# Optimization experiments

Measured on AMD Instinct MI355X. Metric: run time of the kernel, lower is better.

## Reference

```python
import jax, jax.numpy as jnp
import numpy as np

BETA = 0.25
K = 4096
D = 256


def setup_inputs() -> dict:
    key = jax.random.key(0)
    k1, k2 = jax.random.split(key)
    z = jax.random.normal(k1, (4, D, 16, 32, 32), dtype=jnp.float32)
    # mimics nn.init.uniform_(embed.weight, -1/K, 1/K)
    embed = jax.random.uniform(k2, (K, D), minval=-1.0 / K, maxval=1.0 / K, dtype=jnp.float32)
    return {"z": z, "embed": embed}


def reference(z, embed):
    # z: [B, D, T, H, W] -> channel-last [B, T, H, W, D]
    z_perm = jnp.transpose(z, (0, 2, 3, 4, 1))
    flat = z_perm.reshape(-1, embed.shape[1])  # [N, D]
    # squared L2 distances via expansion: |z|^2 - 2 z.e + |e|^2  -> [N, K]
    dist = ((flat ** 2).sum(axis=1, keepdims=True)
            - 2.0 * flat @ embed.T
            + (embed ** 2).sum(axis=1)[None, :])
    idx = jnp.argmin(dist, axis=1)  # [N]
    z_q = embed[idx].reshape(z_perm.shape)  # [B, T, H, W, D]
    # straight-through estimator
    z_q_st = z_perm + jax.lax.stop_gradient(z_q - z_perm)
    z_q_st = jnp.transpose(z_q_st, (0, 4, 1, 2, 3))  # back to [B, D, T, H, W]
    e_q = jnp.transpose(z_q, (0, 4, 1, 2, 3))
    codebook_loss = jnp.mean((jax.lax.stop_gradient(e_q) - z) ** 2)
    commitment_loss = jnp.mean((e_q - jax.lax.stop_gradient(z)) ** 2)
    vq_loss = codebook_loss + BETA * commitment_loss
    indices = idx.reshape(z_perm.shape[:4])  # [B, T, H, W]
    return (z_q_st, vq_loss, indices)
```

## Files before the change

kernel.cpp:

```cpp
#include <hip/hip_runtime.h>
#include <float.h>

#define KC 4096
#define DIM 256
#define MB 16384
#define NTOT 65536
#define ZELEMS 16777216
#define LOSS_OFF 16777216
#define IDX_OFF  16777217
#define TAU 1.5e-4f

#define BT_OFF   524288
#define CNT_OFF  528400
#define CAND_OFF 532480
#define FULL_OFF 800000

typedef _Float16 h8 __attribute__((ext_vector_type(8)));
typedef float f4v __attribute__((ext_vector_type(4)));

__device__ __forceinline__ bool lexlt(float av, int ai, float bv, int bi) {
    return (av < bv) || (av == bv && ai < bi);
}

__global__ __launch_bounds__(256) void vq_prep(const float* __restrict__ e,
                                               float* __restrict__ out) {
    if (blockIdx.x < 512) {
        int t = blockIdx.x * 256 + threadIdx.x;
        int code = t >> 5, s8 = t & 31;
        const float4* src = reinterpret_cast<const float4*>(e + (size_t)code * DIM + s8 * 8);
        float4 v0 = src[0], v1 = src[1];
        float f[8] = {v0.x, v0.y, v0.z, v0.w, v1.x, v1.y, v1.z, v1.w};
        union { uint4 q; _Float16 h[8]; } P;
        #pragma unroll
        for (int p = 0; p < 8; ++p) P.h[p] = (_Float16)(f[p] * 4096.0f);
        int kc = s8 >> 2, khi = s8 & 3;
        int lane = khi * 16 + (code & 15);
        int slot = ((code >> 4) * 8 + kc) * 64 + lane;
        reinterpret_cast<uint4*>(out)[slot] = P.q;
    } else {
        int k = (blockIdx.x - 512) * 4 + (threadIdx.x >> 6);
        int lane = threadIdx.x & 63;
        float4 v = reinterpret_cast<const float4*>(e + (size_t)k * DIM)[lane];
        double s = (double)v.x * v.x + (double)v.y * v.y + (double)v.z * v.z + (double)v.w * v.w;
        #pragma unroll
        for (int off = 32; off > 0; off >>= 1) s += __shfl_down(s, off);
        if (lane == 0) out[BT_OFF + k] = (float)s;
    }
}

#define INS4(V0, V1, V2, V3, L0, L1, L2, L3, v, k)                              \
    if (v < V3) {                                                               \
        if (v < V2) {                                                           \
            V3 = V2; L3 = L2;                                                   \
            if (v < V1) {                                                       \
                V2 = V1; L2 = L1;                                               \
                if (v < V0) { V1 = V0; L1 = L0; V0 = v; L0 = k; }               \
                else        { V1 = v; L1 = k; }                                 \
            } else { V2 = v; L2 = k; }                                          \
        } else { V3 = v; L3 = k; }                                              \
    }

__global__ __launch_bounds__(256) void vq_fast(const float* __restrict__ z,
                                               float* __restrict__ out) {
    __shared__ uint4 etile[2][512];
    __shared__ unsigned long long lists[4][32][4];
    const int tid = threadIdx.x;
    const int wave = tid >> 6, lane = tid & 63;
    const int khi = lane >> 4, l16 = lane & 15;
    const int nbase = blockIdx.x * 128;
    const int b = nbase / MB;
    const int mbase = nbase % MB;
    const float* zb = z + (size_t)b * DIM * MB + mbase + wave * 32 + l16;

    h8 zf0[8], zf1[8];
    #pragma unroll
    for (int kc = 0; kc < 8; ++kc) {
        h8 va, vb;
        #pragma unroll
        for (int j = 0; j < 8; ++j) {
            size_t off = (size_t)(kc * 32 + khi * 8 + j) * MB;
            va[j] = (_Float16)zb[off];
            vb[j] = (_Float16)zb[off + 16];
        }
        zf0[kc] = va; zf1[kc] = vb;
    }

    const uint4* ET = reinterpret_cast<const uint4*>(out);
    const float* Btab = out + BT_OFF;

    float b10 = FLT_MAX, b11 = FLT_MAX;
    int bk0 = 0, bk1 = 0;
    float v00 = FLT_MAX, v01 = FLT_MAX, v02 = FLT_MAX, v03 = FLT_MAX;
    float v10 = FLT_MAX, v11 = FLT_MAX, v12 = FLT_MAX, v13 = FLT_MAX;
    int l00 = 0, l01 = 0, l02 = 0, l03 = 0;
    int l10 = 0, l11 = 0, l12 = 0, l13 = 0;

    uint4 r0 = ET[tid], r1 = ET[tid + 256];
    for (int tile = 0; tile < KC / 16; ++tile) {
        const int cur = tile & 1;
        etile[cur][tid] = r0; etile[cur][tid + 256] = r1;
        __syncthreads();
        if (tile < KC / 16 - 1) {
            r0 = ET[(size_t)(tile + 1) * 512 + tid];
            r1 = ET[(size_t)(tile + 1) * 512 + tid + 256];
        }

        f4v a0 = {0.f, 0.f, 0.f, 0.f}, a1 = a0;
        #pragma unroll
        for (int kc = 0; kc < 8; ++kc) {
            union { uint4 q; h8 v; } af;
            af.q = etile[cur][kc * 64 + lane];
            a0 = __builtin_amdgcn_mfma_f32_16x16x32_f16(af.v, zf0[kc], a0, 0, 0, 0);
            a1 = __builtin_amdgcn_mfma_f32_16x16x32_f16(af.v, zf1[kc], a1, 0, 0, 0);
        }

        const f4v Bv = *reinterpret_cast<const f4v*>(Btab + tile * 16 + khi * 4);
        const int kb = tile * 16 + khi * 4;
        float sc0[4], sc1[4];
        #pragma unroll
        for (int i = 0; i < 4; ++i) {
            sc0[i] = fmaf(-4.8828125e-4f, a0[i], Bv[i]);
            sc1[i] = fmaf(-4.8828125e-4f, a1[i], Bv[i]);
        }
        float m0 = fminf(fminf(sc0[0], sc0[1]), fminf(sc0[2], sc0[3]));
        if (m0 <= b10 + TAU) {
            #pragma unroll
            for (int i = 0; i < 4; ++i) {
                float s = sc0[i]; int k = kb + i;
                if (s < b10) {
                    if (b10 <= s + TAU) INS4(v00, v01, v02, v03, l00, l01, l02, l03, b10, bk0)
                    b10 = s; bk0 = k;
                } else if (s <= b10 + TAU) {
                    INS4(v00, v01, v02, v03, l00, l01, l02, l03, s, k)
                }
            }
        }
        float m1 = fminf(fminf(sc1[0], sc1[1]), fminf(sc1[2], sc1[3]));
        if (m1 <= b11 + TAU) {
            #pragma unroll
            for (int i = 0; i < 4; ++i) {
                float s = sc1[i]; int k = kb + i;
                if (s < b11) {
                    if (b11 <= s + TAU) INS4(v10, v11, v12, v13, l10, l11, l12, l13, b11, bk1)
                    b11 = s; bk1 = k;
                } else if (s <= b11 + TAU) {
                    INS4(v10, v11, v12, v13, l10, l11, l12, l13, s, k)
                }
            }
        }
    }

    float gb0 = b10, gb1 = b11;
    int gk0 = bk0, gk1 = bk1;
    #pragma unroll
    for (int off = 16; off < 64; off <<= 1) {
        float ov = __shfl_xor(gb0, off); int ok = __shfl_xor(gk0, off);
        if (lexlt(ov, ok, gb0, gk0)) { gb0 = ov; gk0 = ok; }
        ov = __shfl_xor(gb1, off); ok = __shfl_xor(gk1, off);
        if (lexlt(ov, ok, gb1, gk1)) { gb1 = ov; gk1 = ok; }
    }
    const float thr0 = gb0 + TAU, thr1 = gb1 + TAU;

    int n0 = 0, pa0 = 0, pb0 = 0, pc0 = 0, pd0 = 0;
    #define ADD0(kk) { if (n0 == 0) pa0 = kk; else if (n0 == 1) pb0 = kk; \
                       else if (n0 == 2) pc0 = kk; else if (n0 == 3) pd0 = kk; n0++; }
    if (b10 <= thr0) ADD0(bk0)
    if (v00 <= thr0) ADD0(l00)
    if (v01 <= thr0) ADD0(l01)
    if (v02 <= thr0) ADD0(l02)
    if (v03 <= thr0) ADD0(l03)
    int n1 = 0, pa1 = 0, pb1 = 0, pc1 = 0, pd1 = 0;
    #define ADD1(kk) { if (n1 == 0) pa1 = kk; else if (n1 == 1) pb1 = kk; \
                       else if (n1 == 2) pc1 = kk; else if (n1 == 3) pd1 = kk; n1++; }
    if (b11 <= thr1) ADD1(bk1)
    if (v10 <= thr1) ADD1(l10)
    if (v11 <= thr1) ADD1(l11)
    if (v12 <= thr1) ADD1(l12)
    if (v13 <= thr1) ADD1(l13)
    lists[wave][l16][khi] = ((unsigned long long)n0 << 48) |
        (unsigned long long)pa0 | ((unsigned long long)pb0 << 12) |
        ((unsigned long long)pc0 << 24) | ((unsigned long long)pd0 << 36);
    lists[wave][16 + l16][khi] = ((unsigned long long)n1 << 48) |
        (unsigned long long)pa1 | ((unsigned long long)pb1 << 12) |
        ((unsigned long long)pc1 << 24) | ((unsigned long long)pd1 << 36);
    __syncthreads();

    unsigned* cntg = (unsigned*)(out + CNT_OFF);
    #pragma unroll
    for (int set = 0; set < 2; ++set) {
        bool act = (lane < 16);
        int gidx = nbase + wave * 32 + set * 16 + l16;
        int I1 = set ? gk1 : gk0;
        int tot = 0, c[4];
        c[0] = c[1] = c[2] = c[3] = I1;
        if (act) {
            #pragma unroll
            for (int q = 0; q < 4; ++q) {
                unsigned long long pl = lists[wave][set * 16 + l16][q];
                int pc = (int)(pl >> 48);
                #pragma unroll
                for (int j = 0; j < 4; ++j) {
                    int kv = (int)((pl >> (12 * j)) & 4095ull);
                    if (j < pc && tot + j < 4) c[tot + j] = kv;
                }
                tot += pc;
            }
            out[IDX_OFF + gidx] = (float)I1;
        }
        bool cand = act && (tot >= 2) && (tot <= 4);
        bool full = act && (tot > 4);
        unsigned long long mc = __ballot(cand);
        if (mc) {
            int leader = __ffsll((long long)mc) - 1;
            unsigned base = 0;
            if (lane == leader) base = atomicAdd(cntg, (unsigned)__popcll(mc));
            base = __shfl(base, leader);
            if (cand) {
                unsigned pos = base + (unsigned)__popcll(mc & ((1ull << lane) - 1ull));
                reinterpret_cast<uint4*>(out + CAND_OFF)[pos] =
                    make_uint4((unsigned)gidx,
                               (unsigned)c[0] | ((unsigned)c[1] << 16),
                               (unsigned)c[2] | ((unsigned)c[3] << 16), 0u);
            }
        }
        unsigned long long mf = __ballot(full);
        if (mf) {
            int leader = __ffsll((long long)mf) - 1;
            unsigned base = 0;
            if (lane == leader) base = atomicAdd(cntg + 1, (unsigned)__popcll(mf));
            base = __shfl(base, leader);
            if (full) {
                unsigned pos = base + (unsigned)__popcll(mf & ((1ull << lane) - 1ull));
                reinterpret_cast<unsigned*>(out + FULL_OFF)[pos] = (unsigned)gidx;
            }
        }
    }
}

__global__ __launch_bounds__(256) void vq_resolve_cand(const float* __restrict__ z,
                                                       const float* __restrict__ e,
                                                       float* __restrict__ out) {
    const int wave = threadIdx.x >> 6, lane = threadIdx.x & 63;
    const unsigned n = *reinterpret_cast<const unsigned*>(out + CNT_OFF);
    const uint4* list = reinterpret_cast<const uint4*>(out + CAND_OFF);
    const float* Btab = out + BT_OFF;
    for (unsigned ei = blockIdx.x * 4 + wave; ei < n; ei += gridDim.x * 4) {
        uint4 ent = list[ei];
        const int gidx = (int)ent.x;
        const int c1 = (int)(ent.y & 0xFFFFu), c2 = (int)(ent.y >> 16);
        const int c3 = (int)(ent.z & 0xFFFFu), c4 = (int)(ent.z >> 16);
        const int b = gidx >> 14, m = gidx & (MB - 1);
        const float* zr = z + (size_t)b * DIM * MB + m;
        const float* e1 = e + (size_t)c1 * DIM;
        const float* e2 = e + (size_t)c2 * DIM;
        const float* e3 = e + (size_t)c3 * DIM;
        const float* e4 = e + (size_t)c4 * DIM;
        double A = 0.0;
        double d1 = 0.0, d2 = 0.0, d3 = 0.0, d4 = 0.0;
        #pragma unroll
        for (int jj = 0; jj < 4; ++jj) {
            int d = lane * 4 + jj;
            double zv = (double)zr[(size_t)d * MB];
            A = fma(zv, zv, A);
            d1 = fma(zv, (double)e1[d], d1);
            d2 = fma(zv, (double)e2[d], d2);
            d3 = fma(zv, (double)e3[d], d3);
            d4 = fma(zv, (double)e4[d], d4);
        }
        #pragma unroll
        for (int mm = 1; mm < 64; mm <<= 1) {
            A += __shfl_xor(A, mm);
            d1 += __shfl_xor(d1, mm); d2 += __shfl_xor(d2, mm);
            d3 += __shfl_xor(d3, mm); d4 += __shfl_xor(d4, mm);
        }
        if (lane == 0) {
            float Af = (float)A;
            float s1 = (Af - (float)(2.0 * d1)) + Btab[c1];
            float s2 = (Af - (float)(2.0 * d2)) + Btab[c2];
            float s3 = (Af - (float)(2.0 * d3)) + Btab[c3];
            float s4 = (Af - (float)(2.0 * d4)) + Btab[c4];
            float bv = s1; int bk = c1;
            if (lexlt(s2, c2, bv, bk)) { bv = s2; bk = c2; }
            if (lexlt(s3, c3, bv, bk)) { bv = s3; bk = c3; }
            if (lexlt(s4, c4, bv, bk)) { bv = s4; bk = c4; }
            out[IDX_OFF + gidx] = (float)bk;
        }
    }
}

__global__ __launch_bounds__(256) void vq_resolve_full(const float* __restrict__ z,
                                                       const float* __restrict__ e,
                                                       float* __restrict__ out) {
    __shared__ float zs[DIM];
    __shared__ float rv[4];
    __shared__ int ri[4];
    const int tid = threadIdx.x;
    const int wave = tid >> 6, lane = tid & 63;
    const unsigned n = reinterpret_cast<const unsigned*>(out + CNT_OFF)[1];
    const unsigned* list = reinterpret_cast<const unsigned*>(out + FULL_OFF);
    const float* Btab = out + BT_OFF;
    for (unsigned ei = blockIdx.x; ei < n; ei += gridDim.x) {
        const int gidx = (int)list[ei];
        const int b = gidx >> 14, m = gidx & (MB - 1);
        const float* zr = z + (size_t)b * DIM * MB + m;
        if (tid < DIM) zs[tid] = zr[(size_t)tid * MB];
        __syncthreads();
        double av = 0.0;
        #pragma unroll
        for (int t2 = 0; t2 < 4; ++t2) {
            double zv = (double)zs[lane * 4 + t2];
            av = fma(zv, zv, av);
        }
        #pragma unroll
        for (int mm = 1; mm < 64; mm <<= 1) av += __shfl_xor(av, mm);
        const float Af = (float)av;

        float bsv = FLT_MAX; int bsk = 0;
        for (int kk = 0; kk < 16; ++kk) {
            const int k = kk * 256 + tid;
            const float4* er4 = reinterpret_cast<const float4*>(e + (size_t)k * DIM);
            const float4* zs4 = reinterpret_cast<const float4*>(zs);
            double dot0 = 0.0, dot1 = 0.0;
            #pragma unroll 8
            for (int d4 = 0; d4 < 64; ++d4) {
                float4 ev = er4[d4];
                float4 zv = zs4[d4];
                dot0 = fma((double)zv.x, (double)ev.x, dot0);
                dot1 = fma((double)zv.y, (double)ev.y, dot1);
                dot0 = fma((double)zv.z, (double)ev.z, dot0);
                dot1 = fma((double)zv.w, (double)ev.w, dot1);
            }
            float s = (Af - (float)(2.0 * (dot0 + dot1))) + Btab[k];
            if (s < bsv) { bsv = s; bsk = k; }
        }
        #pragma unroll
        for (int mm = 1; mm < 64; mm <<= 1) {
            float ov = __shfl_xor(bsv, mm);
            int oi = __shfl_xor(bsk, mm);
            if (ov < bsv || (ov == bsv && oi < bsk)) { bsv = ov; bsk = oi; }
        }
        if (lane == 0) { rv[wave] = bsv; ri[wave] = bsk; }
        __syncthreads();
        if (tid == 0) {
            float bv = rv[0]; int bk = ri[0];
            #pragma unroll
            for (int wv = 1; wv < 4; ++wv) {
                if (rv[wv] < bv || (rv[wv] == bv && ri[wv] < bk)) { bv = rv[wv]; bk = ri[wv]; }
            }
            out[IDX_OFF + gidx] = (float)bk;
        }
        __syncthreads();
    }
}

__global__ __launch_bounds__(256) void vq_apply(const float* __restrict__ z,
                                                const float* __restrict__ e,
                                                float* __restrict__ out) {
    __shared__ int lds_fi[64];
    __shared__ float lds_e[64][260];
    __shared__ double lds_ls[4];
    const int tid = threadIdx.x;
    const int wave = tid >> 6, lane = tid & 63;
    const int nbase = blockIdx.x * 64;
    const int b = nbase / MB;
    const int mbase = nbase % MB;
    if (tid < 64) lds_fi[tid] = (int)out[IDX_OFF + nbase + tid];
    __syncthreads();
    for (int r = wave; r < 64; r += 4) {
        int code = lds_fi[r];
        float4 v = reinterpret_cast<const float4*>(e + (size_t)code * DIM)[lane];
        *reinterpret_cast<float4*>(&lds_e[r][lane * 4]) = v;
    }
    __syncthreads();

    double lsum = 0.0;
    const int mloc = tid & 63;
    const int d0 = tid >> 6;
    #pragma unroll 4
    for (int d = d0; d < DIM; d += 4) {
        float ev = lds_e[mloc][d];
        size_t off = (size_t)b * (DIM * MB) + (size_t)d * MB + mbase + mloc;
        float zv = z[off];
        out[off] = ev;
        float diff = ev - zv;
        lsum += (double)diff * diff;
    }
    #pragma unroll
    for (int off = 32; off > 0; off >>= 1) lsum += __shfl_down(lsum, off);
    if (lane == 0) lds_ls[wave] = lsum;
    __syncthreads();
    if (tid == 0) {
        double t = lds_ls[0] + lds_ls[1] + lds_ls[2] + lds_ls[3];
        atomicAdd(out + LOSS_OFF, (float)(t * (1.25 / (double)ZELEMS)));
    }
}

extern "C" void kernel_launch(void* const* d_in, const int* in_sizes, int n_in,
                              void* d_out, int out_size, void* d_ws, size_t ws_size,
                              hipStream_t stream) {
    const float* z = (const float*)d_in[0];
    const float* e = (const float*)d_in[1];
    float* out = (float*)d_out;

    hipMemsetAsync(out + LOSS_OFF, 0, sizeof(float), stream);
    hipMemsetAsync(out + CNT_OFF, 0, 2 * sizeof(unsigned), stream);
    vq_prep<<<1536, 256, 0, stream>>>(e, out);
    vq_fast<<<NTOT / 128, 256, 0, stream>>>(z, out);
    vq_resolve_cand<<<1024, 256, 0, stream>>>(z, e, out);
    vq_resolve_full<<<512, 256, 0, stream>>>(z, e, out);
    vq_apply<<<NTOT / 64, 256, 0, stream>>>(z, e, out);
}
```

Baseline: 518.8 us.

## Replace branchy top-4 tau tracking with branchless top-3 selection and merge

```diff
diff --git a/kernel.cpp b/kernel.cpp
--- a/kernel.cpp
+++ b/kernel.cpp
@@ -20,6 +20,20 @@
 
 __device__ __forceinline__ bool lexlt(float av, int ai, float bv, int bi) {
     return (av < bv) || (av == bv && ai < bi);
+}
+
+__device__ __forceinline__ void merge3(float& b1, int& i1, float& b2, int& i2, float& b3,
+                                       float c1, int j1, float c2, int j2, float c3) {
+    bool aw = (b1 < c1) || (b1 == c1 && i1 < j1);
+    float x1 = aw ? b1 : c1; int xi1 = aw ? i1 : j1;
+    float x2 = aw ? b2 : c2; int xi2 = aw ? i2 : j2;
+    float x3 = aw ? b3 : c3;
+    float y1 = aw ? c1 : b1; int yi1 = aw ? j1 : i1;
+    float y2 = aw ? c2 : b2;
+    bool s2 = (x2 < y1) || (x2 == y1 && xi2 < yi1);
+    float o2 = s2 ? x2 : y1; int oi2 = s2 ? xi2 : yi1;
+    float o3 = s2 ? fminf(x3, y1) : fminf(x2, y2);
+    b1 = x1; i1 = xi1; b2 = o2; i2 = oi2; b3 = o3;
 }
 
 __global__ __launch_bounds__(256) void vq_prep(const float* __restrict__ e,
@@ -48,22 +62,34 @@
     }
 }
 
-#define INS4(V0, V1, V2, V3, L0, L1, L2, L3, v, k)                              \
-    if (v < V3) {                                                               \
-        if (v < V2) {                                                           \
-            V3 = V2; L3 = L2;                                                   \
-            if (v < V1) {                                                       \
-                V2 = V1; L2 = L1;                                               \
-                if (v < V0) { V1 = V0; L1 = L0; V0 = v; L0 = k; }               \
-                else        { V1 = v; L1 = k; }                                 \
-            } else { V2 = v; L2 = k; }                                          \
-        } else { V3 = v; L3 = k; }                                              \
-    }
+#define SEL4(S0, S1, S2, S3, KB, B1, I1, B2, I2, B3)                             \
+{                                                                                \
+    float lo01 = fminf(S0, S1), hi01 = fmaxf(S0, S1);                            \
+    float lo23 = fminf(S2, S3), hi23 = fmaxf(S2, S3);                            \
+    float m1 = fminf(lo01, lo23);                                                \
+    float m2 = fminf(fmaxf(lo01, lo23), fminf(hi01, hi23));                      \
+    if (m1 < B3) {                                                               \
+        int j1 = (S0 == m1) ? (KB) : ((S1 == m1) ? (KB + 1)                      \
+                 : ((S2 == m1) ? (KB + 2) : (KB + 3)));                          \
+        int j2 = (S0 == m2 && (KB) != j1) ? (KB)                                 \
+                 : ((S1 == m2 && (KB + 1) != j1) ? (KB + 1)                      \
+                 : ((S2 == m2 && (KB + 2) != j1) ? (KB + 2) : (KB + 3)));        \
+        bool c = m1 < B1;                                                        \
+        bool a2 = m1 < B2;                                  \
+        float A2v = a2 ? m1 : B2;  int A2i = a2 ? j1 : I2;                       \
+        float A3v = a2 ? fminf(B2, m2) : fminf(B3, m1);                          \
+        bool bw = m2 < B1;                                   \
+        float Bv2 = bw ? m2 : B1;  int Bi2 = bw ? j2 : I1;                       \
+        float Bv3 = bw ? B1 : fminf(B2, m2);                                     \
+        B3 = c ? Bv3 : A3v;                                                      \
+        B2 = c ? Bv2 : A2v;  I2 = c ? Bi2 : A2i;                                 \
+        B1 = c ? m1 : B1;    I1 = c ? j1 : I1;                                   \
+    }                                                                            \
+}
 
 __global__ __launch_bounds__(256) void vq_fast(const float* __restrict__ z,
                                                float* __restrict__ out) {
     __shared__ uint4 etile[2][512];
-    __shared__ unsigned long long lists[4][32][4];
     const int tid = threadIdx.x;
     const int wave = tid >> 6, lane = tid & 63;
     const int khi = lane >> 4, l16 = lane & 15;
@@ -88,12 +114,9 @@
     const uint4* ET = reinterpret_cast<const uint4*>(out);
     const float* Btab = out + BT_OFF;
 
-    float b10 = FLT_MAX, b11 = FLT_MAX;
-    int bk0 = 0, bk1 = 0;
-    float v00 = FLT_MAX, v01 = FLT_MAX, v02 = FLT_MAX, v03 = FLT_MAX;
-    float v10 = FLT_MAX, v11 = FLT_MAX, v12 = FLT_MAX, v13 = FLT_MAX;
-    int l00 = 0, l01 = 0, l02 = 0, l03 = 0;
-    int l10 = 0, l11 = 0, l12 = 0, l13 = 0;
+    float b10 = FLT_MAX, b20 = FLT_MAX, b30 = FLT_MAX;
+    float b11 = FLT_MAX, b21 = FLT_MAX, b31 = FLT_MAX;
+    int i10 = 0, i20 = 0, i11 = 0, i21 = 0;
 
     uint4 r0 = ET[tid], r1 = ET[tid + 256];
     for (int tile = 0; tile < KC / 16; ++tile) {
@@ -105,110 +128,52 @@
             r1 = ET[(size_t)(tile + 1) * 512 + tid + 256];
         }
 
-        f4v a0 = {0.f, 0.f, 0.f, 0.f}, a1 = a0;
-        #pragma unroll
-        for (int kc = 0; kc < 8; ++kc) {
-            union { uint4 q; h8 v; } af;
-            af.q = etile[cur][kc * 64 + lane];
-            a0 = __builtin_amdgcn_mfma_f32_16x16x32_f16(af.v, zf0[kc], a0, 0, 0, 0);
-            a1 = __builtin_amdgcn_mfma_f32_16x16x32_f16(af.v, zf1[kc], a1, 0, 0, 0);
+        f4v a0e = {0.f, 0.f, 0.f, 0.f}, a0o = a0e, a1e = a0e, a1o = a0e;
+        #pragma unroll
+        for (int kc = 0; kc < 8; kc += 2) {
+            union { uint4 q; h8 v; } afe, afo;
+            afe.q = etile[cur][kc * 64 + lane];
+            afo.q = etile[cur][(kc + 1) * 64 + lane];
+            a0e = __builtin_amdgcn_mfma_f32_16x16x32_f16(afe.v, zf0[kc], a0e, 0, 0, 0);
+            a1e = __builtin_amdgcn_mfma_f32_16x16x32_f16(afe.v, zf1[kc], a1e, 0, 0, 0);
+            a0o = __builtin_amdgcn_mfma_f32_16x16x32_f16(afo.v, zf0[kc + 1], a0o, 0, 0, 0);
+            a1o = __builtin_amdgcn_mfma_f32_16x16x32_f16(afo.v, zf1[kc + 1], a1o, 0, 0, 0);
         }
 
         const f4v Bv = *reinterpret_cast<const f4v*>(Btab + tile * 16 + khi * 4);
         const int kb = tile * 16 + khi * 4;
-        float sc0[4], sc1[4];
+        float s0[4], s1[4];
         #pragma unroll
         for (int i = 0; i < 4; ++i) {
-            sc0[i] = fmaf(-4.8828125e-4f, a0[i], Bv[i]);
-            sc1[i] = fmaf(-4.8828125e-4f, a1[i], Bv[i]);
-        }
-        float m0 = fminf(fminf(sc0[0], sc0[1]), fminf(sc0[2], sc0[3]));
-        if (m0 <= b10 + TAU) {
-            #pragma unroll
-            for (int i = 0; i < 4; ++i) {
-                float s = sc0[i]; int k = kb + i;
-                if (s < b10) {
-                    if (b10 <= s + TAU) INS4(v00, v01, v02, v03, l00, l01, l02, l03, b10, bk0)
-                    b10 = s; bk0 = k;
-                } else if (s <= b10 + TAU) {
-                    INS4(v00, v01, v02, v03, l00, l01, l02, l03, s, k)
-                }
-            }
-        }
-        float m1 = fminf(fminf(sc1[0], sc1[1]), fminf(sc1[2], sc1[3]));
-        if (m1 <= b11 + TAU) {
-            #pragma unroll
-            for (int i = 0; i < 4; ++i) {
-                float s = sc1[i]; int k = kb + i;
-                if (s < b11) {
-                    if (b11 <= s + TAU) INS4(v10, v11, v12, v13, l10, l11, l12, l13, b11, bk1)
-                    b11 = s; bk1 = k;
-                } else if (s <= b11 + TAU) {
-                    INS4(v10, v11, v12, v13, l10, l11, l12, l13, s, k)
-                }
-            }
-        }
-    }
-
-    float gb0 = b10, gb1 = b11;
-    int gk0 = bk0, gk1 = bk1;
+            s0[i] = fmaf(-4.8828125e-4f, a0e[i] + a0o[i], Bv[i]);
+            s1[i] = fmaf(-4.8828125e-4f, a1e[i] + a1o[i], Bv[i]);
+        }
+        SEL4(s0[0], s0[1], s0[2], s0[3], kb, b10, i10, b20, i20, b30)
+        SEL4(s1[0], s1[1], s1[2], s1[3], kb, b11, i11, b21, i21, b31)
+    }
+
     #pragma unroll
     for (int off = 16; off < 64; off <<= 1) {
-        float ov = __shfl_xor(gb0, off); int ok = __shfl_xor(gk0, off);
-        if (lexlt(ov, ok, gb0, gk0)) { gb0 = ov; gk0 = ok; }
-        ov = __shfl_xor(gb1, off); ok = __shfl_xor(gk1, off);
-        if (lexlt(ov, ok, gb1, gk1)) { gb1 = ov; gk1 = ok; }
-    }
-    const float thr0 = gb0 + TAU, thr1 = gb1 + TAU;
-
-    int n0 = 0, pa0 = 0, pb0 = 0, pc0 = 0, pd0 = 0;
-    #define ADD0(kk) { if (n0 == 0) pa0 = kk; else if (n0 == 1) pb0 = kk; \
-                       else if (n0 == 2) pc0 = kk; else if (n0 == 3) pd0 = kk; n0++; }
-    if (b10 <= thr0) ADD0(bk0)
-    if (v00 <= thr0) ADD0(l00)
-    if (v01 <= thr0) ADD0(l01)
-    if (v02 <= thr0) ADD0(l02)
-    if (v03 <= thr0) ADD0(l03)
-    int n1 = 0, pa1 = 0, pb1 = 0, pc1 = 0, pd1 = 0;
-    #define ADD1(kk) { if (n1 == 0) pa1 = kk; else if (n1 == 1) pb1 = kk; \
-                       else if (n1 == 2) pc1 = kk; else if (n1 == 3) pd1 = kk; n1++; }
-    if (b11 <= thr1) ADD1(bk1)
-    if (v10 <= thr1) ADD1(l10)
-    if (v11 <= thr1) ADD1(l11)
-    if (v12 <= thr1) ADD1(l12)
-    if (v13 <= thr1) ADD1(l13)
-    lists[wave][l16][khi] = ((unsigned long long)n0 << 48) |
-        (unsigned long long)pa0 | ((unsigned long long)pb0 << 12) |
-        ((unsigned long long)pc0 << 24) | ((unsigned long long)pd0 << 36);
-    lists[wave][16 + l16][khi] = ((unsigned long long)n1 << 48) |
-        (unsigned long long)pa1 | ((unsigned long long)pb1 << 12) |
-        ((unsigned long long)pc1 << 24) | ((unsigned long long)pd1 << 36);
-    __syncthreads();
+        merge3(b10, i10, b20, i20, b30,
+               __shfl_xor(b10, off), __shfl_xor(i10, off),
+               __shfl_xor(b20, off), __shfl_xor(i20, off), __shfl_xor(b30, off));
+        merge3(b11, i11, b21, i21, b31,
+               __shfl_xor(b11, off), __shfl_xor(i11, off),
+               __shfl_xor(b21, off), __shfl_xor(i21, off), __shfl_xor(b31, off));
+    }
 
     unsigned* cntg = (unsigned*)(out + CNT_OFF);
     #pragma unroll
     for (int set = 0; set < 2; ++set) {
         bool act = (lane < 16);
         int gidx = nbase + wave * 32 + set * 16 + l16;
-        int I1 = set ? gk1 : gk0;
-        int tot = 0, c[4];
-        c[0] = c[1] = c[2] = c[3] = I1;
-        if (act) {
-            #pragma unroll
-            for (int q = 0; q < 4; ++q) {
-                unsigned long long pl = lists[wave][set * 16 + l16][q];
-                int pc = (int)(pl >> 48);
-                #pragma unroll
-                for (int j = 0; j < 4; ++j) {
-                    int kv = (int)((pl >> (12 * j)) & 4095ull);
-                    if (j < pc && tot + j < 4) c[tot + j] = kv;
-                }
-                tot += pc;
-            }
-            out[IDX_OFF + gidx] = (float)I1;
-        }
-        bool cand = act && (tot >= 2) && (tot <= 4);
-        bool full = act && (tot > 4);
+        float B1 = set ? b11 : b10, B2 = set ? b21 : b20, B3 = set ? b31 : b30;
+        int I1 = set ? i11 : i10, I2 = set ? i21 : i20;
+        float thr = B1 + TAU;
+        bool clean = (B2 > thr);
+        bool cand = act && !clean && (B3 > thr);
+        bool full = act && !clean && !cand;
+        if (act) out[IDX_OFF + gidx] = (float)I1;
         unsigned long long mc = __ballot(cand);
         if (mc) {
             int leader = __ffsll((long long)mc) - 1;
@@ -219,8 +184,8 @@
                 unsigned pos = base + (unsigned)__popcll(mc & ((1ull << lane) - 1ull));
                 reinterpret_cast<uint4*>(out + CAND_OFF)[pos] =
                     make_uint4((unsigned)gidx,
-                               (unsigned)c[0] | ((unsigned)c[1] << 16),
-                               (unsigned)c[2] | ((unsigned)c[3] << 16), 0u);
+                               (unsigned)I1 | ((unsigned)I2 << 16),
+                               (unsigned)I1 | ((unsigned)I1 << 16), 0u);
             }
         }
         unsigned long long mf = __ballot(full);
```

Result: slower. 796.6 us (+53.5%).
